# Performance work log

Measured on AMD Instinct MI355X. Metric: run time of the kernel, lower is better.

The kernel has to match this reference:

```python
import jax, jax.numpy as jnp
import numpy as np

N_NODES = 25000
N_EDGES = 400000
ATOM_DIM = 39
EDGE_DIM = 10
FP = 128


def setup_inputs() -> dict:
    key = jax.random.key(0)
    ks = iter(jax.random.split(key, 40))
    def rn(shape, scale=0.1):
        return (jax.random.normal(next(ks), shape, dtype=jnp.float32) * scale)
    inp = {
        'x': jax.random.normal(next(ks), (N_NODES, ATOM_DIM), dtype=jnp.float32),
        'edge_index': jax.random.randint(next(ks), (2, N_EDGES), 0, N_NODES, dtype=jnp.int32),
        'edge_attr': jax.random.normal(next(ks), (N_EDGES, EDGE_DIM), dtype=jnp.float32),
        # layer 0 (step=0): atom_fc + neighbor_fc + align/attend/GRU
        'l0_atom_fc_w': rn((FP, ATOM_DIM)), 'l0_atom_fc_b': rn((FP,)),
        'l0_neighbor_fc_w': rn((FP, ATOM_DIM + EDGE_DIM)), 'l0_neighbor_fc_b': rn((FP,)),
        'l0_align_w': rn((1, 2 * FP)), 'l0_align_b': rn((1,)),
        'l0_attend_w': rn((FP, FP)), 'l0_attend_b': rn((FP,)),
        'l0_w_ih': rn((3 * FP, FP)), 'l0_w_hh': rn((3 * FP, FP)),
        'l0_b_ih': rn((3 * FP,)), 'l0_b_hh': rn((3 * FP,)),
        # layer 1 (step=1): align/attend/GRU only
        'l1_align_w': rn((1, 2 * FP)), 'l1_align_b': rn((1,)),
        'l1_attend_w': rn((FP, FP)), 'l1_attend_b': rn((FP,)),
        'l1_w_ih': rn((3 * FP, FP)), 'l1_w_hh': rn((3 * FP, FP)),
        'l1_b_ih': rn((3 * FP,)), 'l1_b_hh': rn((3 * FP,)),
    }
    return inp


def _lrelu(v):
    return jax.nn.leaky_relu(v, negative_slope=0.01)


def _gru_cell(inp, h, w_ih, w_hh, b_ih, b_hh):
    # torch.nn.GRUCell math
    gi = inp @ w_ih.T + b_ih
    gh = h @ w_hh.T + b_hh
    i_r, i_z, i_n = jnp.split(gi, 3, axis=-1)
    h_r, h_z, h_n = jnp.split(gh, 3, axis=-1)
    r = jax.nn.sigmoid(i_r + h_r)
    z = jax.nn.sigmoid(i_z + h_z)
    n = jnp.tanh(i_n + r * h_n)
    return (1.0 - z) * n + z * h


def _segment_softmax(e, idx, num_segments):
    # PyG torch_geometric.utils.softmax: per-segment max-shifted exp / (sum + 1e-16)
    m = jax.ops.segment_max(e, idx, num_segments=num_segments)
    ex = jnp.exp(e - m[idx])
    s = jax.ops.segment_sum(ex, idx, num_segments=num_segments)
    return ex / (s[idx] + 1e-16)


def _edge_block(x_i, x_j, src, dst, n_nodes, aw, ab, tw, tb, w_ih, w_hh, b_ih, b_hh):
    # align -> segment softmax (keyed by source index, as in the torch code) -> attend -> GRU -> scatter-add
    evu = _lrelu(jnp.concatenate([x_i, x_j], axis=-1) @ aw.T + ab)      # [E,1]
    avu = _segment_softmax(evu, src, n_nodes)                            # [E,1]
    c = jax.nn.elu(avu * (x_i @ tw.T + tb))                              # [E,FP]; dropout is identity in eval
    h = _gru_cell(c, x_i, w_ih, w_hh, b_ih, b_hh)                        # [E,FP]
    return jax.ops.segment_sum(h, dst, num_segments=n_nodes)            # [N,FP] default 'add' aggregation


def reference(x, edge_index, edge_attr,
              l0_atom_fc_w, l0_atom_fc_b, l0_neighbor_fc_w, l0_neighbor_fc_b,
              l0_align_w, l0_align_b, l0_attend_w, l0_attend_b,
              l0_w_ih, l0_w_hh, l0_b_ih, l0_b_hh,
              l1_align_w, l1_align_b, l1_attend_w, l1_attend_b,
              l1_w_ih, l1_w_hh, l1_b_ih, l1_b_hh):
    src, dst = edge_index[0], edge_index[1]   # PyG flow source_to_target: x_j=x[src], x_i=x[dst]
    n_nodes = x.shape[0]
    # --- layer 0 (step == 0) ---
    x_i = _lrelu(x[dst] @ l0_atom_fc_w.T + l0_atom_fc_b)
    x_j = _lrelu(jnp.concatenate([x[src], edge_attr], axis=-1) @ l0_neighbor_fc_w.T + l0_neighbor_fc_b)
    x = _edge_block(x_i, x_j, src, dst, n_nodes,
                    l0_align_w, l0_align_b, l0_attend_w, l0_attend_b,
                    l0_w_ih, l0_w_hh, l0_b_ih, l0_b_hh)
    # --- layer 1 (step == 1) ---
    x_i = x[dst]
    x_j = x[src]
    x = _edge_block(x_i, x_j, src, dst, n_nodes,
                    l1_align_w, l1_align_b, l1_attend_w, l1_attend_b,
                    l1_w_ih, l1_w_hh, l1_b_ih, l1_b_hh)
    return x
```

## Files before the change

### kernel.cpp

```cpp
#include <hip/hip_runtime.h>
#include <hip/hip_bf16.h>
#include <math.h>

#define NN 25000
#define NE 400000

typedef __attribute__((ext_vector_type(8))) short bf16x8;
typedef __attribute__((ext_vector_type(4))) float f32x4;

__device__ __forceinline__ float lrelu(float x){ return x > 0.f ? x : 0.01f*x; }
__device__ __forceinline__ float elu1(float x){ return x > 0.f ? x : (__expf(x)-1.f); }
__device__ __forceinline__ float sigm(float x){ return 1.f/(1.f+__expf(-x)); }
__device__ __forceinline__ float tanh_fast(float x){ float e=__expf(2.f*x); return 1.f - 2.f/(e+1.f); }
__device__ __forceinline__ unsigned fenc(float f){ unsigned u=__float_as_uint(f); return (u&0x80000000u)? ~u : (u|0x80000000u); }
__device__ __forceinline__ float fdec(unsigned k){ return __uint_as_float((k&0x80000000u)? (k^0x80000000u) : ~k); }
__device__ __forceinline__ short f2bf(float f){
    union { float f; unsigned u; } v; v.f = f;
    unsigned r = v.u + 0x7fff + ((v.u >> 16) & 1);
    return (short)(r >> 16);
}
__device__ __forceinline__ float bf2f(short s){
    union { unsigned u; float f; } v; v.u = ((unsigned)(unsigned short)s) << 16;
    return v.f;
}

__global__ __launch_bounds__(256) void k_pack(const float* __restrict__ w,
                                              short* __restrict__ out, int total)
{
    int idx = blockIdx.x*256 + threadIdx.x;
    if (idx < total){
        int i    = idx & 7;
        int lane = (idx >> 3) & 63;
        int ks   = (idx >> 9) & 3;
        int tile = idx >> 11;
        int row  = tile*16 + (lane & 15);
        int k    = ks*32 + ((lane >> 4) << 3) + i;
        out[idx] = f2bf(w[row*128 + k]);
    }
}

__global__ __launch_bounds__(256) void k_hist(const int* __restrict__ dst, unsigned* __restrict__ hist)
{
    int e = blockIdx.x*256 + threadIdx.x;
    if (e < NE) atomicAdd(&hist[dst[e]], 1u);
}

__global__ __launch_bounds__(1024) void k_scan(const unsigned* __restrict__ hist,
                                               unsigned* __restrict__ cursor)
{
    __shared__ unsigned ps[1024];
    const int t = threadIdx.x;
    unsigned loc[25]; unsigned sum = 0;
    const int base = t*25;
    #pragma unroll
    for (int i=0;i<25;i++){ int n=base+i; unsigned v=(n<NN)?hist[n]:0u; loc[i]=sum; sum+=v; }
    ps[t]=sum; __syncthreads();
    for (int off=1; off<1024; off<<=1){
        unsigned v = (t>=off)? ps[t-off] : 0u;
        __syncthreads();
        ps[t] += v;
        __syncthreads();
    }
    unsigned bex = (t==0)? 0u : ps[t-1];
    #pragma unroll
    for (int i=0;i<25;i++){ int n=base+i; if(n<NN) cursor[n] = bex + loc[i]; }
}

__global__ __launch_bounds__(256) void k_scatter(const int* __restrict__ dst,
                                                 unsigned* __restrict__ cursor,
                                                 int* __restrict__ se_id, int* __restrict__ se_dst)
{
    int e = blockIdx.x*256 + threadIdx.x;
    if (e < NE){
        int d = dst[e];
        unsigned p = atomicAdd(&cursor[d], 1u);
        se_id[p]  = e;
        se_dst[p] = d;
    }
}

__global__ __launch_bounds__(256) void k_l0_node(
    const float* __restrict__ x,
    const float* __restrict__ wa, const float* __restrict__ ba,
    const float* __restrict__ wn, const float* __restrict__ bn,
    const float* __restrict__ aw,
    short* __restrict__ A16, short* __restrict__ B16, float* __restrict__ di)
{
    __shared__ float xs[32][40];
    __shared__ float As[32][130];
    const int t = threadIdx.x;
    const int base = blockIdx.x * 32;
    for (int idx = t; idx < 32*39; idx += 256){
        int nn = idx / 39, k = idx - nn*39;
        int node = base + nn;
        xs[nn][k] = (node < NN) ? x[(size_t)node*39 + k] : 0.f;
    }
    __syncthreads();
    const int j = t & 127;
    const int g = t >> 7;
    {
        float accA[16], accB[16];
        #pragma unroll
        for (int nn=0; nn<16; ++nn){ accA[nn]=0.f; accB[nn]=0.f; }
        for (int k=0; k<39; ++k){
            float wva = wa[j*39+k];
            float wvb = wn[j*49+k];
            #pragma unroll
            for (int nn=0; nn<16; ++nn){
                float xv = xs[g*16+nn][k];
                accA[nn] += xv*wva;
                accB[nn] += xv*wvb;
            }
        }
        float bav = ba[j], bnv = bn[j];
        #pragma unroll
        for (int nn=0; nn<16; ++nn){
            int node = base + g*16 + nn;
            float av = lrelu(accA[nn] + bav);
            As[g*16+nn][j] = av;
            if (node < NN){
                A16[(size_t)node*128 + j] = f2bf(av);
                B16[(size_t)node*128 + j] = f2bf(accB[nn] + bnv);
            }
        }
    }
    __syncthreads();
    if (t < 32){
        int node = base + t;
        if (node < NN){
            float d = 0.f;
            for (int k=0; k<128; ++k) d += As[t][k]*aw[k];
            di[node] = d;
        }
    }
}

__global__ __launch_bounds__(256) void k_l1_node(
    const float* __restrict__ x1, const float* __restrict__ aw,
    float* __restrict__ di, float* __restrict__ dj, short* __restrict__ x16)
{
    const int node = blockIdx.x*4 + (threadIdx.x >> 6);
    const int lane = threadIdx.x & 63;
    if (node < NN){
        float v0 = x1[(size_t)node*128 + lane];
        float v1 = x1[(size_t)node*128 + 64 + lane];
        x16[(size_t)node*128 + lane]      = f2bf(v0);
        x16[(size_t)node*128 + 64 + lane] = f2bf(v1);
        float pa = v0*aw[lane]     + v1*aw[64+lane];
        float pb = v0*aw[128+lane] + v1*aw[192+lane];
        #pragma unroll
        for (int off=32; off; off>>=1){ pa += __shfl_xor(pa, off); pb += __shfl_xor(pb, off); }
        if (lane == 0){ di[node] = pa; dj[node] = pb; }
    }
}

__global__ __launch_bounds__(512) void k_node_prep(
    const short* __restrict__ A16,
    const short* __restrict__ twp, const float* __restrict__ tb,
    const short* __restrict__ whhp, const float* __restrict__ bhh,
    short* __restrict__ T16, short* __restrict__ GH16)
{
    __shared__ __align__(16) char A_lds[64*272];
    const int t = threadIdx.x;
    const int base = blockIdx.x << 6;
    #pragma unroll
    for (int it=0; it<2; ++it){
        int cid = it*512 + t;
        int row = cid >> 4, ch = cid & 15;
        int node = base + row; if (node >= NN) node = NN-1;
        *(int4*)(A_lds + row*272 + ch*16) = *(const int4*)(A16 + (size_t)node*128 + ch*8);
    }
    __syncthreads();
    const int w = t >> 6, lane = t & 63;
    const int l15 = lane & 15, lhi = lane >> 4;
    const int jb = w*16 + l15;
    f32x4 Tacc[4], gh[4][3];
    {
        float tbv = tb[jb];
        #pragma unroll
        for (int m=0; m<4; ++m) Tacc[m] = (f32x4){tbv, tbv, tbv, tbv};
        #pragma unroll
        for (int g=0; g<3; ++g){
            float bv = bhh[g*128 + jb];
            #pragma unroll
            for (int m=0; m<4; ++m) gh[m][g] = (f32x4){bv, bv, bv, bv};
        }
    }
    #pragma unroll
    for (int ks=0; ks<4; ++ks){
        bf16x8 af[4];
        #pragma unroll
        for (int m=0; m<4; ++m)
            af[m] = *(const bf16x8*)(A_lds + (m*16+l15)*272 + ks*64 + (lhi<<4));
        bf16x8 tf = *(const bf16x8*)(twp + (size_t)((w*4 + ks)*64 + lane)*8);
        #pragma unroll
        for (int m=0; m<4; ++m)
            Tacc[m] = __builtin_amdgcn_mfma_f32_16x16x32_bf16(af[m], tf, Tacc[m], 0, 0, 0);
        #pragma unroll
        for (int g=0; g<3; ++g){
            bf16x8 wf = *(const bf16x8*)(whhp + (size_t)(((g*8+w)*4 + ks)*64 + lane)*8);
            #pragma unroll
            for (int m=0; m<4; ++m)
                gh[m][g] = __builtin_amdgcn_mfma_f32_16x16x32_bf16(af[m], wf, gh[m][g], 0, 0, 0);
        }
    }
    #pragma unroll
    for (int m=0; m<4; ++m){
        #pragma unroll
        for (int reg=0; reg<4; ++reg){
            int node = base + m*16 + lhi*4 + reg;
            if (node < NN){
                T16[(size_t)node*128 + jb]        = f2bf(Tacc[m][reg]);
                GH16[(size_t)node*384 + jb]       = f2bf(gh[m][0][reg]);
                GH16[(size_t)node*384 + 128 + jb] = f2bf(gh[m][1][reg]);
                GH16[(size_t)node*384 + 256 + jb] = f2bf(gh[m][2][reg]);
            }
        }
    }
}

#define EPW 8
__global__ __launch_bounds__(256) void k_l0_align(
    const int* __restrict__ srcA, const int* __restrict__ dstA,
    const float* __restrict__ ea,
    const short* __restrict__ B16,
    const float* __restrict__ wn,
    const float* __restrict__ aw, const float* __restrict__ ab,
    const float* __restrict__ di,
    float* __restrict__ evu, unsigned* __restrict__ m)
{
    const int t = threadIdx.x;
    const int lane = t & 63;
    const int w = t >> 6;
    float wn2a[10], wn2b[10];
    #pragma unroll
    for (int k=0; k<10; ++k){
        wn2a[k] = wn[lane*49 + 39 + k];
        wn2b[k] = wn[(lane+64)*49 + 39 + k];
    }
    const float awa = aw[128+lane], awb = aw[128+64+lane];
    const float abv = ab[0];
    const int e0 = (blockIdx.x*4 + w) * EPW;
    for (int i=0; i<EPW; ++i){
        int e = e0 + i;
        int s = srcA[e];
        int d = dstA[e];
        float v1 = bf2f(B16[(size_t)s*128 + lane]);
        float v2 = bf2f(B16[(size_t)s*128 + 64 + lane]);
        #pragma unroll
        for (int k=0; k<10; ++k){
            float ev = ea[(size_t)e*10 + k];
            v1 += ev*wn2a[k];
            v2 += ev*wn2b[k];
        }
        v1 = lrelu(v1); v2 = lrelu(v2);
        float p = v1*awa + v2*awb;
        #pragma unroll
        for (int off=32; off; off>>=1) p += __shfl_xor(p, off);
        if (lane == 0){
            float ev = lrelu(p + di[d] + abv);
            evu[e] = ev;
            atomicMax(m + s, fenc(ev));
        }
    }
}

__global__ __launch_bounds__(256) void k_l1_align(
    const int* __restrict__ srcA, const int* __restrict__ dstA,
    const float* __restrict__ di, const float* __restrict__ dj,
    const float* __restrict__ ab,
    float* __restrict__ evu, unsigned* __restrict__ m)
{
    int e = blockIdx.x*256 + threadIdx.x;
    if (e < NE){
        int s = srcA[e], d = dstA[e];
        float v = lrelu(di[d] + dj[s] + ab[0]);
        evu[e] = v;
        atomicMax(m + s, fenc(v));
    }
}

__global__ __launch_bounds__(256) void k_norm(
    const int* __restrict__ srcA, const unsigned* __restrict__ m,
    float* __restrict__ ex, float* __restrict__ s)
{
    int e = blockIdx.x*256 + threadIdx.x;
    if (e < NE){
        int sn = srcA[e];
        float v = __expf(ex[e] - fdec(m[sn]));
        ex[e] = v;
        atomicAdd(s + sn, v);
    }
}

__global__ __launch_bounds__(512) void k_edge_gru(
    const int* __restrict__ srcA,
    const int* __restrict__ se_id, const int* __restrict__ se_dst,
    const float* __restrict__ exA, const float* __restrict__ sA,
    const short* __restrict__ T16, const short* __restrict__ GH16,
    const short* __restrict__ HP16,
    const short* __restrict__ wihp, const float* __restrict__ bih,
    float* __restrict__ out)
{
    __shared__ __align__(16) char smem[64*132*4];
    __shared__ int dsts[64];
    __shared__ float av[64];
    char* const c_lds = smem;
    const int t = threadIdx.x;
    const int p0 = blockIdx.x << 6;
    if (t < 64){
        int p = p0 + t;
        int eid = se_id[p];
        dsts[t] = se_dst[p];
        av[t] = exA[eid] / (sA[srcA[eid]] + 1e-16f);
    }
    __syncthreads();
    #pragma unroll
    for (int it=0; it<2; ++it){
        int cid = it*512 + t;
        int row = cid >> 4, ch = cid & 15;
        int d = dsts[row];
        float a = av[row];
        bf16x8 tv = *(const bf16x8*)(T16 + (size_t)d*128 + ch*8);
        union { short s[8]; int4 v; } u;
        #pragma unroll
        for (int i=0; i<8; ++i) u.s[i] = f2bf(elu1(a * bf2f(tv[i])));
        *(int4*)(c_lds + row*272 + ch*16) = u.v;
    }
    __syncthreads();
    const int w = t >> 6, lane = t & 63;
    const int l15 = lane & 15, lhi = lane >> 4;
    const int jb = w*16 + l15;
    f32x4 gi[4][3];
    #pragma unroll
    for (int g=0; g<3; ++g){
        float bv = bih[g*128 + jb];
        #pragma unroll
        for (int m=0; m<4; ++m) gi[m][g] = (f32x4){bv, bv, bv, bv};
    }
    #pragma unroll
    for (int ks=0; ks<4; ++ks){
        bf16x8 cf[4];
        #pragma unroll
        for (int m=0; m<4; ++m)
            cf[m] = *(const bf16x8*)(c_lds + (m*16+l15)*272 + ks*64 + (lhi<<4));
        #pragma unroll
        for (int g=0; g<3; ++g){
            bf16x8 wf = *(const bf16x8*)(wihp + (size_t)(((g*8+w)*4 + ks)*64 + lane)*8);
            #pragma unroll
            for (int m=0; m<4; ++m)
                gi[m][g] = __builtin_amdgcn_mfma_f32_16x16x32_bf16(cf[m], wf, gi[m][g], 0, 0, 0);
        }
    }
    float hreg[4][4];
    #pragma unroll
    for (int m=0; m<4; ++m){
        #pragma unroll
        for (int reg=0; reg<4; ++reg){
            int e = m*16 + lhi*4 + reg;
            int d = dsts[e];
            const short* gh = GH16 + (size_t)d*384;
            float r = sigm(gi[m][0][reg] + bf2f(gh[jb]));
            float z = sigm(gi[m][1][reg] + bf2f(gh[128+jb]));
            float n = tanh_fast(gi[m][2][reg] + r*bf2f(gh[256+jb]));
            float hp = bf2f(HP16[(size_t)d*128 + jb]);
            hreg[m][reg] = (1.f - z)*n + z*hp;
        }
    }
    __syncthreads();
    {
        float* hlds = (float*)smem;
        #pragma unroll
        for (int m=0; m<4; ++m){
            #pragma unroll
            for (int reg=0; reg<4; ++reg){
                int e = m*16 + lhi*4 + reg;
                hlds[e*132 + jb] = hreg[m][reg];
            }
        }
    }
    __syncthreads();
    {
        const int j = t & 127, eg = t >> 7;
        const float* hlds = (const float*)smem;
        float acc = 0.f; int prev = -1;
        #pragma unroll
        for (int el=0; el<16; ++el){
            int e = eg*16 + el;
            int d = dsts[e];
            float v = hlds[e*132 + j];
            if (d == prev) acc += v;
            else {
                if (prev >= 0) atomicAdd(out + (size_t)prev*128 + j, acc);
                acc = v; prev = d;
            }
        }
        atomicAdd(out + (size_t)prev*128 + j, acc);
    }
}

extern "C" void kernel_launch(void* const* d_in, const int* in_sizes, int n_in,
                              void* d_out, int out_size, void* d_ws, size_t ws_size,
                              hipStream_t stream) {
    const float* x    = (const float*)d_in[0];
    const int*   eidx = (const int*)d_in[1];
    const int*   esrc = eidx;
    const int*   edst = eidx + NE;
    const float* ea   = (const float*)d_in[2];
    const float* a_w  = (const float*)d_in[3];
    const float* a_b  = (const float*)d_in[4];
    const float* n_w  = (const float*)d_in[5];
    const float* n_b  = (const float*)d_in[6];
    const float* al_w0= (const float*)d_in[7];
    const float* al_b0= (const float*)d_in[8];
    const float* t_w0 = (const float*)d_in[9];
    const float* t_b0 = (const float*)d_in[10];
    const float* wih0 = (const float*)d_in[11];
    const float* whh0 = (const float*)d_in[12];
    const float* bih0 = (const float*)d_in[13];
    const float* bhh0 = (const float*)d_in[14];
    const float* al_w1= (const float*)d_in[15];
    const float* al_b1= (const float*)d_in[16];
    const float* t_w1 = (const float*)d_in[17];
    const float* t_b1 = (const float*)d_in[18];
    const float* wih1 = (const float*)d_in[19];
    const float* whh1 = (const float*)d_in[20];
    const float* bih1 = (const float*)d_in[21];
    const float* bhh1 = (const float*)d_in[22];

    float* ws   = (float*)d_ws;
    float* out0 = ws;
    unsigned* m0 = (unsigned*)(out0 + (size_t)NN*128);
    float*    s0 = (float*)(m0 + NN);
    unsigned* m1 = (unsigned*)(s0 + NN);
    float*    s1 = (float*)(m1 + NN);
    float* evu  = s1 + NN;
    float* di   = evu + NE;
    float* dj   = di + NN;
    unsigned* hist   = (unsigned*)(dj + NN);
    unsigned* cursor = hist + NN;
    int* se_id  = (int*)(cursor + NN);
    int* se_dst = se_id + NE;
    short* A16  = (short*)(se_dst + NE);
    short* BX16 = A16 + (size_t)NN*128;
    short* T16  = BX16 + (size_t)NN*128;
    short* GH16 = T16 + (size_t)NN*128;
    short* wp0  = GH16 + (size_t)NN*384;
    short* wp1  = wp0 + 49152;
    short* wh0p = wp1 + 49152;
    short* wh1p = wh0p + 49152;
    short* tp0  = wh1p + 49152;
    short* tp1  = tp0 + 16384;

    hipMemsetAsync(out0, 0, ((size_t)NN*128 + 4*(size_t)NN)*sizeof(float), stream);
    hipMemsetAsync(d_out, 0, (size_t)NN*128*sizeof(float), stream);
    hipMemsetAsync(hist, 0, (size_t)NN*sizeof(unsigned), stream);

    dim3 blk(256);
    k_pack<<<dim3(192), blk, 0, stream>>>(wih0, wp0, 49152);
    k_pack<<<dim3(192), blk, 0, stream>>>(wih1, wp1, 49152);
    k_pack<<<dim3(192), blk, 0, stream>>>(whh0, wh0p, 49152);
    k_pack<<<dim3(192), blk, 0, stream>>>(whh1, wh1p, 49152);
    k_pack<<<dim3(64),  blk, 0, stream>>>(t_w0, tp0, 16384);
    k_pack<<<dim3(64),  blk, 0, stream>>>(t_w1, tp1, 16384);
    k_hist<<<dim3((NE+255)/256), blk, 0, stream>>>(edst, hist);
    k_scan<<<dim3(1), dim3(1024), 0, stream>>>(hist, cursor);
    k_scatter<<<dim3((NE+255)/256), blk, 0, stream>>>(edst, cursor, se_id, se_dst);
    k_l0_node<<<dim3((NN+31)/32), blk, 0, stream>>>(x, a_w, a_b, n_w, n_b, al_w0,
                                                    A16, BX16, di);
    k_node_prep<<<dim3((NN+63)/64), dim3(512), 0, stream>>>(A16, tp0, t_b0, wh0p, bhh0, T16, GH16);
    k_l0_align<<<dim3(NE/(4*EPW)), blk, 0, stream>>>(esrc, edst, ea, BX16, n_w, al_w0, al_b0, di, evu, m0);
    k_norm<<<dim3((NE+255)/256), blk, 0, stream>>>(esrc, m0, evu, s0);
    k_edge_gru<<<dim3(NE/64), dim3(512), 0, stream>>>(esrc, se_id, se_dst, evu, s0,
                                                      T16, GH16, A16, wp0, bih0, out0);
    k_l1_node<<<dim3((NN+3)/4), blk, 0, stream>>>(out0, al_w1, di, dj, BX16);
    k_node_prep<<<dim3((NN+63)/64), dim3(512), 0, stream>>>(BX16, tp1, t_b1, wh1p, bhh1, T16, GH16);
    k_l1_align<<<dim3((NE+255)/256), blk, 0, stream>>>(esrc, edst, di, dj, al_b1, evu, m1);
    k_norm<<<dim3((NE+255)/256), blk, 0, stream>>>(esrc, m1, evu, s1);
    k_edge_gru<<<dim3(NE/64), dim3(512), 0, stream>>>(esrc, se_id, se_dst, evu, s1,
                                                      T16, GH16, BX16, wp1, bih1, (float*)d_out);
}
```

Measured before the change: 719.3 us.

## Replace atomic segment softmax with source-CSR per-node softmax and fuse prep kernels

Builds a second CSR sorted by source node plus an inverse map from edge to its dst-sorted position. The segment softmax then runs per source node inside a single wavefront, with an online max/sum for nodes with more than 64 edges. This replaces the atomicMax/atomicAdd align and norm passes and writes normalized attention directly in dst-sorted order, so the GRU kernel no longer does an indirect gather and divide. It also merges the six weight-pack launches into one and fuses the layer-1 node conversion with node_prep. The cost is extra scatter atomics and index arrays, plus serial per-edge work inside each wave for layer 0.

```diff
diff --git a/kernel.cpp b/kernel.cpp
--- a/kernel.cpp
+++ b/kernel.cpp
@@ -1,9 +1,9 @@
 #include <hip/hip_runtime.h>
-#include <hip/hip_bf16.h>
 #include <math.h>
 
 #define NN 25000
 #define NE 400000
+#define NINF -1e30f
 
 typedef __attribute__((ext_vector_type(8))) short bf16x8;
 typedef __attribute__((ext_vector_type(4))) float f32x4;
@@ -12,8 +12,6 @@
 __device__ __forceinline__ float elu1(float x){ return x > 0.f ? x : (__expf(x)-1.f); }
 __device__ __forceinline__ float sigm(float x){ return 1.f/(1.f+__expf(-x)); }
 __device__ __forceinline__ float tanh_fast(float x){ float e=__expf(2.f*x); return 1.f - 2.f/(e+1.f); }
-__device__ __forceinline__ unsigned fenc(float f){ unsigned u=__float_as_uint(f); return (u&0x80000000u)? ~u : (u|0x80000000u); }
-__device__ __forceinline__ float fdec(unsigned k){ return __uint_as_float((k&0x80000000u)? (k^0x80000000u) : ~k); }
 __device__ __forceinline__ short f2bf(float f){
     union { float f; unsigned u; } v; v.f = f;
     unsigned r = v.u + 0x7fff + ((v.u >> 16) & 1);
@@ -24,36 +22,57 @@
     return v.f;
 }
 
-__global__ __launch_bounds__(256) void k_pack(const float* __restrict__ w,
-                                              short* __restrict__ out, int total)
-{
-    int idx = blockIdx.x*256 + threadIdx.x;
-    if (idx < total){
-        int i    = idx & 7;
-        int lane = (idx >> 3) & 63;
-        int ks   = (idx >> 9) & 3;
-        int tile = idx >> 11;
-        int row  = tile*16 + (lane & 15);
-        int k    = ks*32 + ((lane >> 4) << 3) + i;
-        out[idx] = f2bf(w[row*128 + k]);
-    }
-}
-
-__global__ __launch_bounds__(256) void k_hist(const int* __restrict__ dst, unsigned* __restrict__ hist)
+__global__ __launch_bounds__(256) void k_pack6(
+    const float* __restrict__ w0, const float* __restrict__ w1,
+    const float* __restrict__ w2, const float* __restrict__ w3,
+    const float* __restrict__ w4, const float* __restrict__ w5,
+    short* __restrict__ o0, short* __restrict__ o1, short* __restrict__ o2,
+    short* __restrict__ o3, short* __restrict__ o4, short* __restrict__ o5)
+{
+    int b = blockIdx.x;
+    const float* w; short* o; int idx;
+    if      (b < 192){ w=w0; o=o0; idx = b*256; }
+    else if (b < 384){ w=w1; o=o1; idx = (b-192)*256; }
+    else if (b < 576){ w=w2; o=o2; idx = (b-384)*256; }
+    else if (b < 768){ w=w3; o=o3; idx = (b-576)*256; }
+    else if (b < 832){ w=w4; o=o4; idx = (b-768)*256; }
+    else             { w=w5; o=o5; idx = (b-832)*256; }
+    idx += threadIdx.x;
+    int i    = idx & 7;
+    int lane = (idx >> 3) & 63;
+    int ks   = (idx >> 9) & 3;
+    int tile = idx >> 11;
+    int row  = tile*16 + (lane & 15);
+    int k    = ks*32 + ((lane >> 4) << 3) + i;
+    o[idx] = f2bf(w[row*128 + k]);
+}
+
+__global__ __launch_bounds__(256) void k_hist2(const int* __restrict__ src,
+                                               const int* __restrict__ dst,
+                                               unsigned* __restrict__ hd,
+                                               unsigned* __restrict__ hs)
 {
     int e = blockIdx.x*256 + threadIdx.x;
-    if (e < NE) atomicAdd(&hist[dst[e]], 1u);
-}
-
-__global__ __launch_bounds__(1024) void k_scan(const unsigned* __restrict__ hist,
-                                               unsigned* __restrict__ cursor)
+    if (e < NE){
+        atomicAdd(&hd[dst[e]], 1u);
+        atomicAdd(&hs[src[e]], 1u);
+    }
+}
+
+__global__ __launch_bounds__(1024) void k_scan2(
+    const unsigned* __restrict__ hd, unsigned* __restrict__ cd,
+    const unsigned* __restrict__ hs, unsigned* __restrict__ cs,
+    int* __restrict__ srcptr)
 {
     __shared__ unsigned ps[1024];
+    const int issrc = blockIdx.x;
+    const unsigned* h = issrc ? hs : hd;
+    unsigned* c = issrc ? cs : cd;
     const int t = threadIdx.x;
     unsigned loc[25]; unsigned sum = 0;
     const int base = t*25;
     #pragma unroll
-    for (int i=0;i<25;i++){ int n=base+i; unsigned v=(n<NN)?hist[n]:0u; loc[i]=sum; sum+=v; }
+    for (int i=0;i<25;i++){ int n=base+i; unsigned v=(n<NN)?h[n]:0u; loc[i]=sum; sum+=v; }
     ps[t]=sum; __syncthreads();
     for (int off=1; off<1024; off<<=1){
         unsigned v = (t>=off)? ps[t-off] : 0u;
@@ -63,19 +82,32 @@
     }
     unsigned bex = (t==0)? 0u : ps[t-1];
     #pragma unroll
-    for (int i=0;i<25;i++){ int n=base+i; if(n<NN) cursor[n] = bex + loc[i]; }
-}
-
-__global__ __launch_bounds__(256) void k_scatter(const int* __restrict__ dst,
-                                                 unsigned* __restrict__ cursor,
-                                                 int* __restrict__ se_id, int* __restrict__ se_dst)
+    for (int i=0;i<25;i++){
+        int n=base+i;
+        if (n<NN){
+            unsigned off = bex + loc[i];
+            c[n] = off;
+            if (issrc) srcptr[n] = (int)off;
+        }
+    }
+    if (issrc && t==1023) srcptr[NN] = NE;
+}
+
+__global__ __launch_bounds__(256) void k_scatter2(
+    const int* __restrict__ src, const int* __restrict__ dst,
+    unsigned* __restrict__ cd, unsigned* __restrict__ cs,
+    int* __restrict__ se_dst, int* __restrict__ inv_dst,
+    int* __restrict__ se2_id, int* __restrict__ se2_dst)
 {
     int e = blockIdx.x*256 + threadIdx.x;
     if (e < NE){
-        int d = dst[e];
-        unsigned p = atomicAdd(&cursor[d], 1u);
-        se_id[p]  = e;
+        int d = dst[e], s = src[e];
+        unsigned p = atomicAdd(&cd[d], 1u);
         se_dst[p] = d;
+        inv_dst[e] = (int)p;
+        unsigned q = atomicAdd(&cs[s], 1u);
+        se2_id[q] = e;
+        se2_dst[q] = d;
     }
 }
 
@@ -135,25 +167,6 @@
     }
 }
 
-__global__ __launch_bounds__(256) void k_l1_node(
-    const float* __restrict__ x1, const float* __restrict__ aw,
-    float* __restrict__ di, float* __restrict__ dj, short* __restrict__ x16)
-{
-    const int node = blockIdx.x*4 + (threadIdx.x >> 6);
-    const int lane = threadIdx.x & 63;
-    if (node < NN){
-        float v0 = x1[(size_t)node*128 + lane];
-        float v1 = x1[(size_t)node*128 + 64 + lane];
-        x16[(size_t)node*128 + lane]      = f2bf(v0);
-        x16[(size_t)node*128 + 64 + lane] = f2bf(v1);
-        float pa = v0*aw[lane]     + v1*aw[64+lane];
-        float pb = v0*aw[128+lane] + v1*aw[192+lane];
-        #pragma unroll
-        for (int off=32; off; off>>=1){ pa += __shfl_xor(pa, off); pb += __shfl_xor(pb, off); }
-        if (lane == 0){ di[node] = pa; dj[node] = pb; }
-    }
-}
-
 __global__ __launch_bounds__(512) void k_node_prep(
     const short* __restrict__ A16,
     const short* __restrict__ twp, const float* __restrict__ tb,
@@ -219,84 +232,268 @@
     }
 }
 
-#define EPW 8
-__global__ __launch_bounds__(256) void k_l0_align(
-    const int* __restrict__ srcA, const int* __restrict__ dstA,
-    const float* __restrict__ ea,
-    const short* __restrict__ B16,
-    const float* __restrict__ wn,
-    const float* __restrict__ aw, const float* __restrict__ ab,
-    const float* __restrict__ di,
-    float* __restrict__ evu, unsigned* __restrict__ m)
-{
+__global__ __launch_bounds__(512) void k_l1_prep(
+    const float* __restrict__ out0, const float* __restrict__ aw,
+    const short* __restrict__ twp, const float* __restrict__ tb,
+    const short* __restrict__ whhp, const float* __restrict__ bhh,
+    short* __restrict__ x16, float* __restrict__ di, float* __restrict__ dj,
+    short* __restrict__ T16, short* __restrict__ GH16)
+{
+    __shared__ __align__(16) char x_lds[64*272];
     const int t = threadIdx.x;
-    const int lane = t & 63;
-    const int w = t >> 6;
+    const int base = blockIdx.x << 6;
+    {
+        int r = t >> 3, c0 = (t & 7) * 16;
+        int node = base + r;
+        int nc = node < NN ? node : NN-1;
+        const float4* sp = (const float4*)(out0 + (size_t)nc*128 + c0);
+        float4 f0 = sp[0], f1 = sp[1], f2 = sp[2], f3 = sp[3];
+        union { short s[16]; int4 v[2]; } u;
+        u.s[0]=f2bf(f0.x); u.s[1]=f2bf(f0.y); u.s[2]=f2bf(f0.z); u.s[3]=f2bf(f0.w);
+        u.s[4]=f2bf(f1.x); u.s[5]=f2bf(f1.y); u.s[6]=f2bf(f1.z); u.s[7]=f2bf(f1.w);
+        u.s[8]=f2bf(f2.x); u.s[9]=f2bf(f2.y); u.s[10]=f2bf(f2.z); u.s[11]=f2bf(f2.w);
+        u.s[12]=f2bf(f3.x); u.s[13]=f2bf(f3.y); u.s[14]=f2bf(f3.z); u.s[15]=f2bf(f3.w);
+        *(int4*)(x_lds + r*272 + c0*2)      = u.v[0];
+        *(int4*)(x_lds + r*272 + c0*2 + 16) = u.v[1];
+        if (node < NN){
+            *(int4*)(x16 + (size_t)node*128 + c0)     = u.v[0];
+            *(int4*)(x16 + (size_t)node*128 + c0 + 8) = u.v[1];
+        }
+    }
+    __syncthreads();
+    const int w = t >> 6, lane = t & 63;
+    {
+        float a0 = aw[lane], a1 = aw[64+lane], a2 = aw[128+lane], a3 = aw[192+lane];
+        for (int i=0;i<8;++i){
+            int r = w*8 + i;
+            int node = base + r;
+            float v0 = bf2f(*(const short*)(x_lds + r*272 + lane*2));
+            float v1 = bf2f(*(const short*)(x_lds + r*272 + 128 + lane*2));
+            float pa = v0*a0 + v1*a1;
+            float pb = v0*a2 + v1*a3;
+            #pragma unroll
+            for (int off=32; off; off>>=1){ pa += __shfl_xor(pa,off); pb += __shfl_xor(pb,off); }
+            if (lane==0 && node<NN){ di[node]=pa; dj[node]=pb; }
+        }
+    }
+    const int l15 = lane & 15, lhi = lane >> 4;
+    const int jb = w*16 + l15;
+    f32x4 Tacc[4], gh[4][3];
+    {
+        float tbv = tb[jb];
+        #pragma unroll
+        for (int m=0; m<4; ++m) Tacc[m] = (f32x4){tbv, tbv, tbv, tbv};
+        #pragma unroll
+        for (int g=0; g<3; ++g){
+            float bv = bhh[g*128 + jb];
+            #pragma unroll
+            for (int m=0; m<4; ++m) gh[m][g] = (f32x4){bv, bv, bv, bv};
+        }
+    }
+    #pragma unroll
+    for (int ks=0; ks<4; ++ks){
+        bf16x8 af[4];
+        #pragma unroll
+        for (int m=0; m<4; ++m)
+            af[m] = *(const bf16x8*)(x_lds + (m*16+l15)*272 + ks*64 + (lhi<<4));
+        bf16x8 tf = *(const bf16x8*)(twp + (size_t)((w*4 + ks)*64 + lane)*8);
+        #pragma unroll
+        for (int m=0; m<4; ++m)
+            Tacc[m] = __builtin_amdgcn_mfma_f32_16x16x32_bf16(af[m], tf, Tacc[m], 0, 0, 0);
+        #pragma unroll
+        for (int g=0; g<3; ++g){
+            bf16x8 wf = *(const bf16x8*)(whhp + (size_t)(((g*8+w)*4 + ks)*64 + lane)*8);
+            #pragma unroll
+            for (int m=0; m<4; ++m)
+                gh[m][g] = __builtin_amdgcn_mfma_f32_16x16x32_bf16(af[m], wf, gh[m][g], 0, 0, 0);
+        }
+    }
+    #pragma unroll
+    for (int m=0; m<4; ++m){
+        #pragma unroll
+        for (int reg=0; reg<4; ++reg){
+            int node = base + m*16 + lhi*4 + reg;
+            if (node < NN){
+                T16[(size_t)node*128 + jb]        = f2bf(Tacc[m][reg]);
+                GH16[(size_t)node*384 + jb]       = f2bf(gh[m][0][reg]);
+                GH16[(size_t)node*384 + 128 + jb] = f2bf(gh[m][1][reg]);
+                GH16[(size_t)node*384 + 256 + jb] = f2bf(gh[m][2][reg]);
+            }
+        }
+    }
+}
+
+__global__ __launch_bounds__(256) void k_align0(
+    const int* __restrict__ srcptr, const int* __restrict__ se2_id,
+    const int* __restrict__ se2_dst, const int* __restrict__ inv_dst,
+    const float* __restrict__ ea, const short* __restrict__ B16,
+    const float* __restrict__ wn, const float* __restrict__ aw,
+    const float* __restrict__ ab, const float* __restrict__ di,
+    float* __restrict__ evu_tmp, float* __restrict__ avu)
+{
+    const int lane = threadIdx.x & 63;
+    const int node = blockIdx.x*4 + (threadIdx.x >> 6);
+    if (node >= NN) return;
+    const int start = srcptr[node], end = srcptr[node+1];
+    if (start >= end) return;
     float wn2a[10], wn2b[10];
     #pragma unroll
-    for (int k=0; k<10; ++k){
+    for (int k=0;k<10;++k){
         wn2a[k] = wn[lane*49 + 39 + k];
         wn2b[k] = wn[(lane+64)*49 + 39 + k];
     }
-    const float awa = aw[128+lane], awb = aw[128+64+lane];
+    const float awa = aw[128+lane], awb = aw[192+lane];
     const float abv = ab[0];
-    const int e0 = (blockIdx.x*4 + w) * EPW;
-    for (int i=0; i<EPW; ++i){
-        int e = e0 + i;
-        int s = srcA[e];
-        int d = dstA[e];
-        float v1 = bf2f(B16[(size_t)s*128 + lane]);
-        float v2 = bf2f(B16[(size_t)s*128 + 64 + lane]);
-        #pragma unroll
-        for (int k=0; k<10; ++k){
-            float ev = ea[(size_t)e*10 + k];
-            v1 += ev*wn2a[k];
-            v2 += ev*wn2b[k];
-        }
-        v1 = lrelu(v1); v2 = lrelu(v2);
-        float p = v1*awa + v2*awb;
-        #pragma unroll
-        for (int off=32; off; off>>=1) p += __shfl_xor(p, off);
-        if (lane == 0){
-            float ev = lrelu(p + di[d] + abv);
-            evu[e] = ev;
-            atomicMax(m + s, fenc(ev));
-        }
-    }
-}
-
-__global__ __launch_bounds__(256) void k_l1_align(
-    const int* __restrict__ srcA, const int* __restrict__ dstA,
+    const float v1b = bf2f(B16[(size_t)node*128 + lane]);
+    const float v2b = bf2f(B16[(size_t)node*128 + 64 + lane]);
+    const int deg = end - start;
+    if (deg <= 64){
+        int myeid = 0; float mydi = 0.f; float ear[10];
+        if (lane < deg){
+            int pos = start + lane;
+            myeid = se2_id[pos];
+            mydi  = di[se2_dst[pos]];
+            #pragma unroll
+            for (int k=0;k<10;++k) ear[k] = ea[(size_t)myeid*10 + k];
+        }
+        float pv = NINF;
+        for (int i=0;i<deg;++i){
+            float v1 = v1b, v2 = v2b;
+            #pragma unroll
+            for (int k=0;k<10;++k){
+                float e = __shfl(ear[k], i);
+                v1 += e*wn2a[k]; v2 += e*wn2b[k];
+            }
+            v1 = lrelu(v1); v2 = lrelu(v2);
+            float p = v1*awa + v2*awb;
+            #pragma unroll
+            for (int off=32; off; off>>=1) p += __shfl_xor(p, off);
+            float pe = lrelu(p + __shfl(mydi, i) + abv);
+            if (lane == i) pv = pe;
+        }
+        float cm = pv;
+        #pragma unroll
+        for (int off=32; off; off>>=1) cm = fmaxf(cm, __shfl_xor(cm, off));
+        float ex = (lane < deg) ? __expf(pv - cm) : 0.f;
+        float cs = ex;
+        #pragma unroll
+        for (int off=32; off; off>>=1) cs += __shfl_xor(cs, off);
+        if (lane < deg) avu[inv_dst[myeid]] = ex / (cs + 1e-16f);
+    } else {
+        float mrun = NINF, srun = 0.f;
+        for (int c0 = start; c0 < end; c0 += 64){
+            int nE = min(64, end - c0);
+            int myeid=0; float mydi=0.f; float ear[10];
+            if (lane < nE){
+                int pos = c0 + lane;
+                myeid = se2_id[pos];
+                mydi = di[se2_dst[pos]];
+                #pragma unroll
+                for (int k=0;k<10;++k) ear[k] = ea[(size_t)myeid*10 + k];
+            }
+            float pv = NINF;
+            for (int i=0;i<nE;++i){
+                float v1=v1b, v2=v2b;
+                #pragma unroll
+                for (int k=0;k<10;++k){
+                    float e = __shfl(ear[k], i);
+                    v1 += e*wn2a[k]; v2 += e*wn2b[k];
+                }
+                v1=lrelu(v1); v2=lrelu(v2);
+                float p = v1*awa + v2*awb;
+                #pragma unroll
+                for (int off=32; off; off>>=1) p += __shfl_xor(p, off);
+                float pe = lrelu(p + __shfl(mydi,i) + abv);
+                if (lane == i) pv = pe;
+            }
+            if (lane < nE) evu_tmp[c0+lane] = pv;
+            float cm = pv;
+            #pragma unroll
+            for (int off=32; off; off>>=1) cm = fmaxf(cm, __shfl_xor(cm,off));
+            float nm = fmaxf(mrun, cm);
+            float exs = (lane<nE)? __expf(pv-nm) : 0.f;
+            float cs = exs;
+            #pragma unroll
+            for (int off=32; off; off>>=1) cs += __shfl_xor(cs, off);
+            srun = srun*__expf(mrun-nm) + cs;
+            mrun = nm;
+        }
+        float inv = 1.f/(srun + 1e-16f);
+        for (int c0 = start; c0 < end; c0 += 64){
+            int nE = min(64, end - c0);
+            if (lane < nE){
+                int pos = c0+lane;
+                float pv = evu_tmp[pos];
+                avu[inv_dst[se2_id[pos]]] = __expf(pv - mrun)*inv;
+            }
+        }
+    }
+}
+
+__global__ __launch_bounds__(256) void k_align1(
+    const int* __restrict__ srcptr, const int* __restrict__ se2_id,
+    const int* __restrict__ se2_dst, const int* __restrict__ inv_dst,
     const float* __restrict__ di, const float* __restrict__ dj,
     const float* __restrict__ ab,
-    float* __restrict__ evu, unsigned* __restrict__ m)
-{
-    int e = blockIdx.x*256 + threadIdx.x;
-    if (e < NE){
-        int s = srcA[e], d = dstA[e];
-        float v = lrelu(di[d] + dj[s] + ab[0]);
-        evu[e] = v;
-        atomicMax(m + s, fenc(v));
-    }
-}
-
-__global__ __launch_bounds__(256) void k_norm(
-    const int* __restrict__ srcA, const unsigned* __restrict__ m,
-    float* __restrict__ ex, float* __restrict__ s)
-{
-    int e = blockIdx.x*256 + threadIdx.x;
-    if (e < NE){
-        int sn = srcA[e];
-        float v = __expf(ex[e] - fdec(m[sn]));
-        ex[e] = v;
-        atomicAdd(s + sn, v);
+    float* __restrict__ evu_tmp, float* __restrict__ avu)
+{
+    const int lane = threadIdx.x & 63;
+    const int node = blockIdx.x*4 + (threadIdx.x >> 6);
+    if (node >= NN) return;
+    const int start = srcptr[node], end = srcptr[node+1];
+    if (start >= end) return;
+    const float djs = dj[node] + ab[0];
+    const int deg = end - start;
+    if (deg <= 64){
+        int myeid = 0; float pv = NINF;
+        if (lane < deg){
+            int pos = start + lane;
+            myeid = se2_id[pos];
+            pv = lrelu(di[se2_dst[pos]] + djs);
+        }
+        float cm = pv;
+        #pragma unroll
+        for (int off=32; off; off>>=1) cm = fmaxf(cm, __shfl_xor(cm, off));
+        float ex = (lane < deg) ? __expf(pv - cm) : 0.f;
+        float cs = ex;
+        #pragma unroll
+        for (int off=32; off; off>>=1) cs += __shfl_xor(cs, off);
+        if (lane < deg) avu[inv_dst[myeid]] = ex / (cs + 1e-16f);
+    } else {
+        float mrun = NINF, srun = 0.f;
+        for (int c0 = start; c0 < end; c0 += 64){
+            int nE = min(64, end - c0);
+            float pv = NINF;
+            if (lane < nE){
+                int pos = c0 + lane;
+                pv = lrelu(di[se2_dst[pos]] + djs);
+                evu_tmp[pos] = pv;
+            }
+            float cm = pv;
+            #pragma unroll
+            for (int off=32; off; off>>=1) cm = fmaxf(cm, __shfl_xor(cm,off));
+            float nm = fmaxf(mrun, cm);
+            float exs = (lane<nE)? __expf(pv-nm) : 0.f;
+            float cs = exs;
+            #pragma unroll
+            for (int off=32; off; off>>=1) cs += __shfl_xor(cs, off);
+            srun = srun*__expf(mrun-nm) + cs;
+            mrun = nm;
+        }
+        float inv = 1.f/(srun + 1e-16f);
+        for (int c0 = start; c0 < end; c0 += 64){
+            int nE = min(64, end - c0);
+            if (lane < nE){
+                int pos = c0+lane;
+                avu[inv_dst[se2_id[pos]]] = __expf(evu_tmp[pos] - mrun)*inv;
+            }
+        }
     }
 }
 
 __global__ __launch_bounds__(512) void k_edge_gru(
-    const int* __restrict__ srcA,
-    const int* __restrict__ se_id, const int* __restrict__ se_dst,
-    const float* __restrict__ exA, const float* __restrict__ sA,
+    const int* __restrict__ se_dst,
+    const float* __restrict__ avu,
     const short* __restrict__ T16, const short* __restrict__ GH16,
     const short* __restrict__ HP16,
     const short* __restrict__ wihp, const float* __restrict__ bih,
@@ -309,10 +506,8 @@
     const int t = threadIdx.x;
     const int p0 = blockIdx.x << 6;
     if (t < 64){
-        int p = p0 + t;
-        int eid = se_id[p];
-        dsts[t] = se_dst[p];
-        av[t] = exA[eid] / (sA[srcA[eid]] + 1e-16f);
+        dsts[t] = se_dst[p0 + t];
+        av[t] = avu[p0 + t];
     }
     __syncthreads();
     #pragma unroll
@@ -430,18 +625,20 @@
 
     float* ws   = (float*)d_ws;
     float* out0 = ws;
-    unsigned* m0 = (unsigned*)(out0 + (size_t)NN*128);
-    float*    s0 = (float*)(m0 + NN);
-    unsigned* m1 = (unsigned*)(s0 + NN);
-    float*    s1 = (float*)(m1 + NN);
-    float* evu  = s1 + NN;
-    float* di   = evu + NE;
+    float* avu  = out0 + (size_t)NN*128;
+    float* evu_tmp = avu + NE;
+    float* di   = evu_tmp + NE;
     float* dj   = di + NN;
-    unsigned* hist   = (unsigned*)(dj + NN);
-    unsigned* cursor = hist + NN;
-    int* se_id  = (int*)(cursor + NN);
-    int* se_dst = se_id + NE;
-    short* A16  = (short*)(se_dst + NE);
+    unsigned* hist_d = (unsigned*)(dj + NN);
+    unsigned* hist_s = hist_d + NN;
+    unsigned* cur_d  = hist_s + NN;
+    unsigned* cur_s  = cur_d + NN;
+    int* srcptr = (int*)(cur_s + NN);
+    int* se_dst  = srcptr + NN + 1;
+    int* inv_dst = se_dst + NE;
+    int* se2_id  = inv_dst + NE;
+    int* se2_dst = se2_id + NE;
+    short* A16  = (short*)(se2_dst + NE);
     short* BX16 = A16 + (size_t)NN*128;
     short* T16  = BX16 + (size_t)NN*128;
     short* GH16 = T16 + (size_t)NN*128;
@@ -452,31 +649,28 @@
     short* tp0  = wh1p + 49152;
     short* tp1  = tp0 + 16384;
 
-    hipMemsetAsync(out0, 0, ((size_t)NN*128 + 4*(size_t)NN)*sizeof(float), stream);
+    hipMemsetAsync(out0, 0, (size_t)NN*128*sizeof(float), stream);
     hipMemsetAsync(d_out, 0, (size_t)NN*128*sizeof(float), stream);
-    hipMemsetAsync(hist, 0, (size_t)NN*sizeof(unsigned), stream);
+    hipMemsetAsync(hist_d, 0, (size_t)2*NN*sizeof(unsigned), stream);
 
     dim3 blk(256);
-    k_pack<<<dim3(192), blk, 0, stream>>>(wih0, wp0, 49152);
-    k_pack<<<dim3(192), blk, 0, stream>>>(wih1, wp1, 49152);
-    k_pack<<<dim3(192), blk, 0, stream>>>(whh0, wh0p, 49152);
-    k_pack<<<dim3(192), blk, 0, stream>>>(whh1, wh1p, 49152);
-    k_pack<<<dim3(64),  blk, 0, stream>>>(t_w0, tp0, 16384);
-    k_pack<<<dim3(64),  blk, 0, stream>>>(t_w1, tp1, 16384);
-    k_hist<<<dim3((NE+255)/256), blk, 0, stream>>>(edst, hist);
-    k_scan<<<dim3(1), dim3(1024), 0, stream>>>(hist, cursor);
-    k_scatter<<<dim3((NE+255)/256), blk, 0, stream>>>(edst, cursor, se_id, se_dst);
+    k_pack6<<<dim3(896), blk, 0, stream>>>(wih0, wih1, whh0, whh1, t_w0, t_w1,
+                                           wp0, wp1, wh0p, wh1p, tp0, tp1);
+    k_hist2<<<dim3((NE+255)/256), blk, 0, stream>>>(esrc, edst, hist_d, hist_s);
+    k_scan2<<<dim3(2), dim3(1024), 0, stream>>>(hist_d, cur_d, hist_s, cur_s, srcptr);
+    k_scatter2<<<dim3((NE+255)/256), blk, 0, stream>>>(esrc, edst, cur_d, cur_s,
+                                                       se_dst, inv_dst, se2_id, se2_dst);
     k_l0_node<<<dim3((NN+31)/32), blk, 0, stream>>>(x, a_w, a_b, n_w, n_b, al_w0,
                                                     A16, BX16, di);
     k_node_prep<<<dim3((NN+63)/64), dim3(512), 0, stream>>>(A16, tp0, t_b0, wh0p, bhh0, T16, GH16);
-    k_l0_align<<<dim3(NE/(4*EPW)), blk, 0, stream>>>(esrc, edst, ea, BX16, n_w, al_w0, al_b0, di, evu, m0);
-    k_norm<<<dim3((NE+255)/256), blk, 0, stream>>>(esrc, m0, evu, s0);
-    k_edge_gru<<<dim3(NE/64), dim3(512), 0, stream>>>(esrc, se_id, se_dst, evu, s0,
-                                                      T16, GH16, A16, wp0, bih0, out0);
-    k_l1_node<<<dim3((NN+3)/4), blk, 0, stream>>>(out0, al_w1, di, dj, BX16);
-    k_node_prep<<<dim3((NN+63)/64), dim3(512), 0, stream>>>(BX16, tp1, t_b1, wh1p, bhh1, T16, GH16);
-    k_l1_align<<<dim3((NE+255)/256), blk, 0, stream>>>(esrc, edst, di, dj, al_b1, evu, m1);
-    k_norm<<<dim3((NE+255)/256), blk, 0, stream>>>(esrc, m1, evu, s1);
-    k_edge_gru<<<dim3(NE/64), dim3(512), 0, stream>>>(esrc, se_id, se_dst, evu, s1,
-                                                      T16, GH16, BX16, wp1, bih1, (float*)d_out);
-}
+    k_align0<<<dim3((NN+3)/4), blk, 0, stream>>>(srcptr, se2_id, se2_dst, inv_dst,
+                                                 ea, BX16, n_w, al_w0, al_b0, di, evu_tmp, avu);
+    k_edge_gru<<<dim3(NE/64), dim3(512), 0, stream>>>(se_dst, avu, T16, GH16, A16,
+                                                      wp0, bih0, out0);
+    k_l1_prep<<<dim3((NN+63)/64), dim3(512), 0, stream>>>(out0, al_w1, tp1, t_b1, wh1p, bhh1,
+                                                          BX16, di, dj, T16, GH16);
+    k_align1<<<dim3((NN+3)/4), blk, 0, stream>>>(srcptr, se2_id, se2_dst, inv_dst,
+                                                 di, dj, al_b1, evu_tmp, avu);
+    k_edge_gru<<<dim3(NE/64), dim3(512), 0, stream>>>(se_dst, avu, T16, GH16, BX16,
+                                                      wp1, bih1, (float*)d_out);
+}
```

Result: faster. 648.4 us (-9.9%).
